# Optimization experiments

Hardware: AMD Instinct MI355X
Metric: run time of the kernel (lower is better)

## Reference

```python
import jax, jax.numpy as jnp
import numpy as np

B, T, C = 2048, 64, 384  # batch, seq (== block_size), n_embd
HEAD = 64


def setup_inputs() -> dict:
    key = jax.random.key(0)
    k1, k2, k3, k4 = jax.random.split(key, 4)
    x = jax.random.normal(k1, (B, T, C), dtype=jnp.float32)
    Wq = jax.random.normal(k2, (C, HEAD), dtype=jnp.float32) * (C ** -0.5)
    Wk = jax.random.normal(k3, (C, HEAD), dtype=jnp.float32) * (C ** -0.5)
    Wv = jax.random.normal(k4, (C, HEAD), dtype=jnp.float32) * (C ** -0.5)
    return {"x": x, "Wq": Wq, "Wk": Wk, "Wv": Wv}


def reference(x, Wq, Wk, Wv):
    Bx, Tx, Cx = x.shape
    q = jnp.einsum('btc,ch->bth', x, Wq)
    k = jnp.einsum('btc,ch->bth', x, Wk)
    v = jnp.einsum('btc,ch->bth', x, Wv)
    # NOTE: original code scales by n_embd**-0.5 (C), not head_size**-0.5
    wei = jnp.einsum('bth,bsh->bts', q, k) * (Cx ** -0.5)
    causal = jnp.tril(jnp.ones((Tx, Tx), dtype=bool))  # tril[:T,:T]
    wei = jnp.where(causal, wei, -jnp.inf)
    wei = jax.nn.softmax(wei, axis=-1)
    # dropout is identity in eval mode
    out = jnp.einsum('bts,bsh->bth', wei, v)
    return out
```

## Files before the change

kernel.cpp:

```cpp
#include <hip/hip_runtime.h>
#include <stdint.h>

typedef _Float16 f16;
typedef _Float16 f16x8 __attribute__((ext_vector_type(8)));
typedef _Float16 f16x4 __attribute__((ext_vector_type(4)));
typedef float floatx4 __attribute__((ext_vector_type(4)));
typedef float floatx2 __attribute__((ext_vector_type(2)));

#define TT 64
#define CDIM 384
#define HH 64
#define NKK 12
#define LDP 72
#define OST 66
#define CHUNK 12288
#define WBUFH 6144
#define ARENA 4608
#define SCALE 0.05103103630798288f

__global__ void prep_w(const float* __restrict__ Wq,
                       const float* __restrict__ Wk,
                       const float* __restrict__ Wv,
                       f16* __restrict__ wf) {
    int t = blockIdx.x * 256 + threadIdx.x;
    if (t >= 3 * NKK * 4 * 64) return;
    int lane = t & 63;
    int tile = (t >> 6) & 3;
    int p    = (t >> 8) % 3;
    int kk   = t / 768;
    const float* W = (p == 0) ? Wq : ((p == 1) ? Wk : Wv);
    int n  = tile * 16 + (lane & 15);
    int k0 = kk * 32 + (lane >> 4) * 8;
    f16x8 frag;
#pragma unroll
    for (int j = 0; j < 8; ++j) frag[j] = (f16)W[(k0 + j) * HH + n];
    ((f16x8*)wf)[t] = frag;
}

static __device__ __forceinline__ f16x8 cvt8(float4 f0, float4 f1) {
    f16x8 h;
    h[0]=(f16)f0.x; h[1]=(f16)f0.y; h[2]=(f16)f0.z; h[3]=(f16)f0.w;
    h[4]=(f16)f1.x; h[5]=(f16)f1.y; h[6]=(f16)f1.z; h[7]=(f16)f1.w;
    return h;
}

static __device__ __forceinline__ void glds16(const void* g, void* l) {
    __builtin_amdgcn_global_load_lds(
        (const __attribute__((address_space(1))) uint32_t*)g,
        (__attribute__((address_space(3))) uint32_t*)l, 16, 0, 0);
}

__launch_bounds__(256, 5)
__global__ void attn_head(const float* __restrict__ x,
                          const f16* __restrict__ wf,
                          float* __restrict__ out) {
    __shared__ __align__(16) char smem[3 * TT * LDP * sizeof(f16)];
    f16* wbuf = (f16*)smem;
    f16* qs   = (f16*)smem;
    f16* ksm  = qs + ARENA;
    f16* vst  = qs + 2 * ARENA;
    f16* ps   = qs;
    float* ost = (float*)smem;

    const int b    = blockIdx.x;
    const int tid  = threadIdx.x;
    const int wave = tid >> 6;
    const int lane = tid & 63;
    const int quad = lane >> 4;
    const int cl   = lane & 15;
    const int row0 = wave * 16;

    const floatx4 fzero = {0.f, 0.f, 0.f, 0.f};
    floatx4 acc[12];
#pragma unroll
    for (int T = 0; T < 12; ++T) acc[T] = fzero;

    const float* xp = x + ((size_t)b * TT + row0 + cl) * CDIM + quad * 8;
    const char* wb  = (const char*)wf;
    const int lslot = (wave * 64 + lane) * 16;

    float4 xa[2], xb[2];
#pragma unroll
    for (int j = 0; j < 3; ++j)
        glds16(wb + j * 4096 + lslot, wbuf + j * 2048 + wave * 512);
    asm volatile("" ::: "memory");
    xa[0] = *(const float4*)(xp);
    xb[0] = *(const float4*)(xp + 4);
    asm volatile("" ::: "memory");

#pragma unroll
    for (int kk = 0; kk < NKK; ++kk) {
        if (kk == NKK - 1) asm volatile("s_waitcnt vmcnt(0)" ::: "memory");
        else               asm volatile("s_waitcnt vmcnt(2)" ::: "memory");
        __builtin_amdgcn_s_barrier();
        if (kk + 1 < NKK) {
            const int nb = (kk + 1) & 1;
#pragma unroll
            for (int j = 0; j < 3; ++j)
                glds16(wb + (kk + 1) * CHUNK + j * 4096 + lslot,
                       wbuf + nb * WBUFH + j * 2048 + wave * 512);
            asm volatile("" ::: "memory");
            xa[nb] = *(const float4*)(xp + (kk + 1) * 32);
            xb[nb] = *(const float4*)(xp + (kk + 1) * 32 + 4);
            asm volatile("" ::: "memory");
        }
        f16x8 xf = cvt8(xa[kk & 1], xb[kk & 1]);
        const f16* wc = wbuf + (kk & 1) * WBUFH;
        __builtin_amdgcn_s_setprio(1);
#pragma unroll
        for (int T = 0; T < 12; ++T) {
            f16x8 bf = *(const f16x8*)&wc[(T * 64 + lane) * 8];
            acc[T] = __builtin_amdgcn_mfma_f32_16x16x32_f16(xf, bf, acc[T], 0, 0, 0);
        }
        __builtin_amdgcn_s_setprio(0);
    }
    __syncthreads();

#pragma unroll
    for (int T = 0; T < 12; ++T) {
        int p = T >> 2;
        int h = (T & 3) * 16 + cl;
        if (p == 2) {
            f16x4 vv;
            vv[0]=(f16)acc[T][0]; vv[1]=(f16)acc[T][1];
            vv[2]=(f16)acc[T][2]; vv[3]=(f16)acc[T][3];
            *(f16x4*)&vst[h * LDP + row0 + quad * 4] = vv;
        } else if (p == 0) {
#pragma unroll
            for (int r = 0; r < 4; ++r)
                qs[(row0 + quad * 4 + r) * LDP + h] = (f16)(acc[T][r] * SCALE);
        } else {
#pragma unroll
            for (int r = 0; r < 4; ++r)
                ksm[(row0 + quad * 4 + r) * LDP + h] = (f16)acc[T][r];
        }
    }
    __syncthreads();

    floatx4 sa[4];
#pragma unroll
    for (int t = 0; t < 4; ++t) sa[t] = fzero;
#pragma unroll
    for (int kv = 0; kv < 2; ++kv) {
        f16x8 aq = *(const f16x8*)&qs[(row0 + cl) * LDP + kv * 32 + quad * 8];
#pragma unroll
        for (int t = 0; t < 4; ++t) {
            f16x8 bk = *(const f16x8*)&ksm[(t * 16 + cl) * LDP + kv * 32 + quad * 8];
            sa[t] = __builtin_amdgcn_mfma_f32_16x16x32_f16(aq, bk, sa[t], 0, 0, 0);
        }
    }
    __syncthreads();

#pragma unroll
    for (int t = 0; t < 4; ++t) {
        int s = t * 16 + cl;
#pragma unroll
        for (int r = 0; r < 4; ++r) {
            int tr = row0 + quad * 4 + r;
            float p = (s <= tr) ? __expf(sa[t][r]) : 0.0f;
            ps[tr * LDP + s] = (f16)p;
        }
    }
    __syncthreads();

    floatx4 oa[4];
    floatx4 den = fzero;
#pragma unroll
    for (int t = 0; t < 4; ++t) oa[t] = fzero;
    f16x8 ones;
#pragma unroll
    for (int j = 0; j < 8; ++j) ones[j] = (f16)1.0f;
#pragma unroll
    for (int kv = 0; kv < 2; ++kv) {
        f16x8 ap = *(const f16x8*)&ps[(row0 + cl) * LDP + kv * 32 + quad * 8];
        den = __builtin_amdgcn_mfma_f32_16x16x32_f16(ap, ones, den, 0, 0, 0);
#pragma unroll
        for (int t = 0; t < 4; ++t) {
            f16x8 bv = *(const f16x8*)&vst[(t * 16 + cl) * LDP + kv * 32 + quad * 8];
            oa[t] = __builtin_amdgcn_mfma_f32_16x16x32_f16(ap, bv, oa[t], 0, 0, 0);
        }
    }
    float rden[4];
#pragma unroll
    for (int r = 0; r < 4; ++r) rden[r] = 1.0f / den[r];
    __syncthreads();

#pragma unroll
    for (int t = 0; t < 4; ++t)
#pragma unroll
        for (int r = 0; r < 4; ++r)
            ost[(row0 + quad * 4 + r) * OST + t * 16 + cl] = oa[t][r] * rden[r];
    __syncthreads();

    float* op = out + (size_t)b * TT * HH;
#pragma unroll
    for (int i = 0; i < 4; ++i) {
        int row = i * 16 + (tid >> 4);
        int c4  = (tid & 15) * 4;
        floatx2 lo = *(const floatx2*)&ost[row * OST + c4];
        floatx2 hi = *(const floatx2*)&ost[row * OST + c4 + 2];
        float4 v; v.x = lo[0]; v.y = lo[1]; v.z = hi[0]; v.w = hi[1];
        *(float4*)&op[row * HH + c4] = v;
    }
}

extern "C" void kernel_launch(void* const* d_in, const int* in_sizes, int n_in,
                              void* d_out, int out_size, void* d_ws, size_t ws_size,
                              hipStream_t stream) {
    const float* x  = (const float*)d_in[0];
    const float* Wq = (const float*)d_in[1];
    const float* Wk = (const float*)d_in[2];
    const float* Wv = (const float*)d_in[3];
    float* out = (float*)d_out;
    f16* wf = (f16*)d_ws;

    prep_w<<<36, 256, 0, stream>>>(Wq, Wk, Wv, wf);
    attn_head<<<2048, 256, 0, stream>>>(x, wf, out);
}
```

Before: 301.3 us.

## Load projection weights directly from global memory instead of LDS staging

New measurement: 330.8 us. 9.8% more time.

```diff
diff --git a/kernel.cpp b/kernel.cpp
--- a/kernel.cpp
+++ b/kernel.cpp
@@ -13,8 +13,6 @@
 #define NKK 12
 #define LDP 72
 #define OST 66
-#define CHUNK 12288
-#define WBUFH 6144
 #define ARENA 4608
 #define SCALE 0.05103103630798288f
 
@@ -44,18 +42,11 @@
     return h;
 }
 
-static __device__ __forceinline__ void glds16(const void* g, void* l) {
-    __builtin_amdgcn_global_load_lds(
-        (const __attribute__((address_space(1))) uint32_t*)g,
-        (__attribute__((address_space(3))) uint32_t*)l, 16, 0, 0);
-}
-
-__launch_bounds__(256, 5)
+__launch_bounds__(256, 4)
 __global__ void attn_head(const float* __restrict__ x,
                           const f16* __restrict__ wf,
                           float* __restrict__ out) {
     __shared__ __align__(16) char smem[3 * TT * LDP * sizeof(f16)];
-    f16* wbuf = (f16*)smem;
     f16* qs   = (f16*)smem;
     f16* ksm  = qs + ARENA;
     f16* vst  = qs + 2 * ARENA;
@@ -76,45 +67,25 @@
     for (int T = 0; T < 12; ++T) acc[T] = fzero;
 
     const float* xp = x + ((size_t)b * TT + row0 + cl) * CDIM + quad * 8;
-    const char* wb  = (const char*)wf;
-    const int lslot = (wave * 64 + lane) * 16;
+    const f16x8* wl = (const f16x8*)wf + lane;
 
-    float4 xa[2], xb[2];
-#pragma unroll
-    for (int j = 0; j < 3; ++j)
-        glds16(wb + j * 4096 + lslot, wbuf + j * 2048 + wave * 512);
-    asm volatile("" ::: "memory");
-    xa[0] = *(const float4*)(xp);
-    xb[0] = *(const float4*)(xp + 4);
-    asm volatile("" ::: "memory");
+    float4 xa = *(const float4*)(xp);
+    float4 xb = *(const float4*)(xp + 4);
 
-#pragma unroll
+#pragma unroll 2
     for (int kk = 0; kk < NKK; ++kk) {
-        if (kk == NKK - 1) asm volatile("s_waitcnt vmcnt(0)" ::: "memory");
-        else               asm volatile("s_waitcnt vmcnt(2)" ::: "memory");
-        __builtin_amdgcn_s_barrier();
+        f16x8 xf = cvt8(xa, xb);
         if (kk + 1 < NKK) {
-            const int nb = (kk + 1) & 1;
-#pragma unroll
-            for (int j = 0; j < 3; ++j)
-                glds16(wb + (kk + 1) * CHUNK + j * 4096 + lslot,
-                       wbuf + nb * WBUFH + j * 2048 + wave * 512);
-            asm volatile("" ::: "memory");
-            xa[nb] = *(const float4*)(xp + (kk + 1) * 32);
-            xb[nb] = *(const float4*)(xp + (kk + 1) * 32 + 4);
-            asm volatile("" ::: "memory");
+            xa = *(const float4*)(xp + (kk + 1) * 32);
+            xb = *(const float4*)(xp + (kk + 1) * 32 + 4);
         }
-        f16x8 xf = cvt8(xa[kk & 1], xb[kk & 1]);
-        const f16* wc = wbuf + (kk & 1) * WBUFH;
-        __builtin_amdgcn_s_setprio(1);
+        const f16x8* wk = wl + kk * 768;
 #pragma unroll
         for (int T = 0; T < 12; ++T) {
-            f16x8 bf = *(const f16x8*)&wc[(T * 64 + lane) * 8];
+            f16x8 bf = wk[T * 64];
             acc[T] = __builtin_amdgcn_mfma_f32_16x16x32_f16(xf, bf, acc[T], 0, 0, 0);
         }
-        __builtin_amdgcn_s_setprio(0);
     }
-    __syncthreads();
 
 #pragma unroll
     for (int T = 0; T < 12; ++T) {
@@ -149,7 +120,6 @@
             sa[t] = __builtin_amdgcn_mfma_f32_16x16x32_f16(aq, bk, sa[t], 0, 0, 0);
         }
     }
-    __syncthreads();
 
 #pragma unroll
     for (int t = 0; t < 4; ++t) {
@@ -161,7 +131,6 @@
             ps[tr * LDP + s] = (f16)p;
         }
     }
-    __syncthreads();
 
     floatx4 oa[4];
     floatx4 den = fzero;
```

## Split fused attention into QKV projection kernel and attention kernel via workspace

Applied to the files above, without the earlier changes.

Measured after the change: 329.1 us. +9.2%, slower.

```diff
diff --git a/kernel.cpp b/kernel.cpp
--- a/kernel.cpp
+++ b/kernel.cpp
@@ -5,18 +5,21 @@
 typedef _Float16 f16x8 __attribute__((ext_vector_type(8)));
 typedef _Float16 f16x4 __attribute__((ext_vector_type(4)));
 typedef float floatx4 __attribute__((ext_vector_type(4)));
-typedef float floatx2 __attribute__((ext_vector_type(2)));
 
 #define TT 64
 #define CDIM 384
 #define HH 64
 #define NKK 12
 #define LDP 72
-#define OST 66
 #define CHUNK 12288
 #define WBUFH 6144
-#define ARENA 4608
 #define SCALE 0.05103103630798288f
+
+#define WF_OFF 0
+#define QF_OFF (256 * 1024)
+#define TENB   (2048 * 64 * 64 * 2)
+#define KF_OFF (QF_OFF + TENB)
+#define VT_OFF (KF_OFF + TENB)
 
 __global__ void prep_w(const float* __restrict__ Wq,
                        const float* __restrict__ Wk,
@@ -50,17 +53,107 @@
         (__attribute__((address_space(3))) uint32_t*)l, 16, 0, 0);
 }
 
-__launch_bounds__(256, 5)
-__global__ void attn_head(const float* __restrict__ x,
-                          const f16* __restrict__ wf,
-                          float* __restrict__ out) {
-    __shared__ __align__(16) char smem[3 * TT * LDP * sizeof(f16)];
-    f16* wbuf = (f16*)smem;
-    f16* qs   = (f16*)smem;
-    f16* ksm  = qs + ARENA;
-    f16* vst  = qs + 2 * ARENA;
-    f16* ps   = qs;
-    float* ost = (float*)smem;
+__launch_bounds__(256, 3)
+__global__ void proj_qkv(const float* __restrict__ x,
+                         const f16* __restrict__ wf,
+                         f16* __restrict__ qf,
+                         f16* __restrict__ kf,
+                         f16* __restrict__ vt) {
+    __shared__ __align__(16) f16 wbuf[2 * WBUFH];
+
+    const int tid  = threadIdx.x;
+    const int wave = tid >> 6;
+    const int lane = tid & 63;
+    const int quad = lane >> 4;
+    const int cl   = lane & 15;
+    const int R0   = blockIdx.x * 128 + wave * 32;
+
+    const floatx4 fzero = {0.f, 0.f, 0.f, 0.f};
+    floatx4 acc[2][12];
+#pragma unroll
+    for (int mi = 0; mi < 2; ++mi)
+#pragma unroll
+        for (int T = 0; T < 12; ++T) acc[mi][T] = fzero;
+
+    const float* xp0 = x + (size_t)(R0 + cl) * CDIM + quad * 8;
+    const float* xp1 = x + (size_t)(R0 + 16 + cl) * CDIM + quad * 8;
+    const char*  wb  = (const char*)wf;
+    const int lslot  = (wave * 64 + lane) * 16;
+
+    float4 xa[2][2], xb[2][2];
+#pragma unroll
+    for (int j = 0; j < 3; ++j)
+        glds16(wb + j * 4096 + lslot, wbuf + j * 2048 + wave * 512);
+    asm volatile("" ::: "memory");
+    xa[0][0] = *(const float4*)(xp0); xb[0][0] = *(const float4*)(xp0 + 4);
+    xa[0][1] = *(const float4*)(xp1); xb[0][1] = *(const float4*)(xp1 + 4);
+    asm volatile("" ::: "memory");
+
+#pragma unroll
+    for (int kk = 0; kk < NKK; ++kk) {
+        asm volatile("s_waitcnt vmcnt(4)" ::: "memory");
+        __builtin_amdgcn_s_barrier();
+        if (kk + 1 < NKK) {
+            const int nb = (kk + 1) & 1;
+#pragma unroll
+            for (int j = 0; j < 3; ++j)
+                glds16(wb + (kk + 1) * CHUNK + j * 4096 + lslot,
+                       wbuf + nb * WBUFH + j * 2048 + wave * 512);
+            asm volatile("" ::: "memory");
+            xa[nb][0] = *(const float4*)(xp0 + (kk + 1) * 32);
+            xb[nb][0] = *(const float4*)(xp0 + (kk + 1) * 32 + 4);
+            xa[nb][1] = *(const float4*)(xp1 + (kk + 1) * 32);
+            xb[nb][1] = *(const float4*)(xp1 + (kk + 1) * 32 + 4);
+            asm volatile("" ::: "memory");
+        }
+        const int cur = kk & 1;
+        f16x8 xf0 = cvt8(xa[cur][0], xb[cur][0]);
+        f16x8 xf1 = cvt8(xa[cur][1], xb[cur][1]);
+        const f16* wc = wbuf + cur * WBUFH;
+        __builtin_amdgcn_s_setprio(1);
+#pragma unroll
+        for (int T = 0; T < 12; ++T) {
+            f16x8 bf = *(const f16x8*)&wc[(T * 64 + lane) * 8];
+            acc[0][T] = __builtin_amdgcn_mfma_f32_16x16x32_f16(xf0, bf, acc[0][T], 0, 0, 0);
+            acc[1][T] = __builtin_amdgcn_mfma_f32_16x16x32_f16(xf1, bf, acc[1][T], 0, 0, 0);
+        }
+        __builtin_amdgcn_s_setprio(0);
+    }
+
+#pragma unroll
+    for (int mi = 0; mi < 2; ++mi) {
+        const int rbase = R0 + mi * 16 + quad * 4;
+#pragma unroll
+        for (int T = 0; T < 12; ++T) {
+            const int p = T >> 2;
+            const int h = (T & 3) * 16 + cl;
+            if (p == 0) {
+#pragma unroll
+                for (int r = 0; r < 4; ++r)
+                    qf[(size_t)(rbase + r) * HH + h] = (f16)(acc[mi][T][r] * SCALE);
+            } else if (p == 1) {
+#pragma unroll
+                for (int r = 0; r < 4; ++r)
+                    kf[(size_t)(rbase + r) * HH + h] = (f16)acc[mi][T][r];
+            } else {
+                const int tb = R0 + mi * 16;
+                const int b  = tb >> 6;
+                const int t0 = (tb & 63) + quad * 4;
+                f16x4 vv;
+                vv[0]=(f16)acc[mi][T][0]; vv[1]=(f16)acc[mi][T][1];
+                vv[2]=(f16)acc[mi][T][2]; vv[3]=(f16)acc[mi][T][3];
+                *(f16x4*)&vt[(size_t)b * 4096 + h * 64 + t0] = vv;
+            }
+        }
+    }
+}
+
+__launch_bounds__(256, 4)
+__global__ void attn_sm(const f16* __restrict__ qf,
+                        const f16* __restrict__ kf,
+                        const f16* __restrict__ vt,
+                        float* __restrict__ out) {
+    __shared__ __align__(16) f16 ps[TT * LDP];
 
     const int b    = blockIdx.x;
     const int tid  = threadIdx.x;
@@ -69,87 +162,28 @@
     const int quad = lane >> 4;
     const int cl   = lane & 15;
     const int row0 = wave * 16;
+    const size_t base = (size_t)b * (TT * HH);
+
+    f16x8 aq[2], bk[4][2], bv[4][2];
+#pragma unroll
+    for (int kv = 0; kv < 2; ++kv) {
+        aq[kv] = *(const f16x8*)&qf[base + (row0 + cl) * HH + kv * 32 + quad * 8];
+#pragma unroll
+        for (int t = 0; t < 4; ++t) {
+            bk[t][kv] = *(const f16x8*)&kf[base + (t * 16 + cl) * HH + kv * 32 + quad * 8];
+            bv[t][kv] = *(const f16x8*)&vt[base + (t * 16 + cl) * HH + kv * 32 + quad * 8];
+        }
+    }
 
     const floatx4 fzero = {0.f, 0.f, 0.f, 0.f};
-    floatx4 acc[12];
-#pragma unroll
-    for (int T = 0; T < 12; ++T) acc[T] = fzero;
-
-    const float* xp = x + ((size_t)b * TT + row0 + cl) * CDIM + quad * 8;
-    const char* wb  = (const char*)wf;
-    const int lslot = (wave * 64 + lane) * 16;
-
-    float4 xa[2], xb[2];
-#pragma unroll
-    for (int j = 0; j < 3; ++j)
-        glds16(wb + j * 4096 + lslot, wbuf + j * 2048 + wave * 512);
-    asm volatile("" ::: "memory");
-    xa[0] = *(const float4*)(xp);
-    xb[0] = *(const float4*)(xp + 4);
-    asm volatile("" ::: "memory");
-
-#pragma unroll
-    for (int kk = 0; kk < NKK; ++kk) {
-        if (kk == NKK - 1) asm volatile("s_waitcnt vmcnt(0)" ::: "memory");
-        else               asm volatile("s_waitcnt vmcnt(2)" ::: "memory");
-        __builtin_amdgcn_s_barrier();
-        if (kk + 1 < NKK) {
-            const int nb = (kk + 1) & 1;
-#pragma unroll
-            for (int j = 0; j < 3; ++j)
-                glds16(wb + (kk + 1) * CHUNK + j * 4096 + lslot,
-                       wbuf + nb * WBUFH + j * 2048 + wave * 512);
-            asm volatile("" ::: "memory");
-            xa[nb] = *(const float4*)(xp + (kk + 1) * 32);
-            xb[nb] = *(const float4*)(xp + (kk + 1) * 32 + 4);
-            asm volatile("" ::: "memory");
-        }
-        f16x8 xf = cvt8(xa[kk & 1], xb[kk & 1]);
-        const f16* wc = wbuf + (kk & 1) * WBUFH;
-        __builtin_amdgcn_s_setprio(1);
-#pragma unroll
-        for (int T = 0; T < 12; ++T) {
-            f16x8 bf = *(const f16x8*)&wc[(T * 64 + lane) * 8];
-            acc[T] = __builtin_amdgcn_mfma_f32_16x16x32_f16(xf, bf, acc[T], 0, 0, 0);
-        }
-        __builtin_amdgcn_s_setprio(0);
-    }
-    __syncthreads();
-
-#pragma unroll
-    for (int T = 0; T < 12; ++T) {
-        int p = T >> 2;
-        int h = (T & 3) * 16 + cl;
-        if (p == 2) {
-            f16x4 vv;
-            vv[0]=(f16)acc[T][0]; vv[1]=(f16)acc[T][1];
-            vv[2]=(f16)acc[T][2]; vv[3]=(f16)acc[T][3];
-            *(f16x4*)&vst[h * LDP + row0 + quad * 4] = vv;
-        } else if (p == 0) {
-#pragma unroll
-            for (int r = 0; r < 4; ++r)
-                qs[(row0 + quad * 4 + r) * LDP + h] = (f16)(acc[T][r] * SCALE);
-        } else {
-#pragma unroll
-            for (int r = 0; r < 4; ++r)
-                ksm[(row0 + quad * 4 + r) * LDP + h] = (f16)acc[T][r];
-        }
-    }
-    __syncthreads();
-
     floatx4 sa[4];
 #pragma unroll
     for (int t = 0; t < 4; ++t) sa[t] = fzero;
 #pragma unroll
-    for (int kv = 0; kv < 2; ++kv) {
-        f16x8 aq = *(const f16x8*)&qs[(row0 + cl) * LDP + kv * 32 + quad * 8];
-#pragma unroll
-        for (int t = 0; t < 4; ++t) {
-            f16x8 bk = *(const f16x8*)&ksm[(t * 16 + cl) * LDP + kv * 32 + quad * 8];
-            sa[t] = __builtin_amdgcn_mfma_f32_16x16x32_f16(aq, bk, sa[t], 0, 0, 0);
-        }
-    }
-    __syncthreads();
+    for (int kv = 0; kv < 2; ++kv)
+#pragma unroll
+        for (int t = 0; t < 4; ++t)
+            sa[t] = __builtin_amdgcn_mfma_f32_16x16x32_f16(aq[kv], bk[t][kv], sa[t], 0, 0, 0);
 
 #pragma unroll
     for (int t = 0; t < 4; ++t) {
@@ -161,7 +195,6 @@
             ps[tr * LDP + s] = (f16)p;
         }
     }
-    __syncthreads();
 
     floatx4 oa[4];
     floatx4 den = fzero;
@@ -175,33 +208,19 @@
         f16x8 ap = *(const f16x8*)&ps[(row0 + cl) * LDP + kv * 32 + quad * 8];
         den = __builtin_amdgcn_mfma_f32_16x16x32_f16(ap, ones, den, 0, 0, 0);
 #pragma unroll
-        for (int t = 0; t < 4; ++t) {
-            f16x8 bv = *(const f16x8*)&vst[(t * 16 + cl) * LDP + kv * 32 + quad * 8];
-            oa[t] = __builtin_amdgcn_mfma_f32_16x16x32_f16(ap, bv, oa[t], 0, 0, 0);
-        }
+        for (int t = 0; t < 4; ++t)
+            oa[t] = __builtin_amdgcn_mfma_f32_16x16x32_f16(ap, bv[t][kv], oa[t], 0, 0, 0);
     }
     float rden[4];
 #pragma unroll
     for (int r = 0; r < 4; ++r) rden[r] = 1.0f / den[r];
-    __syncthreads();
-
+
+    float* op = out + base;
 #pragma unroll
     for (int t = 0; t < 4; ++t)
 #pragma unroll
         for (int r = 0; r < 4; ++r)
-            ost[(row0 + quad * 4 + r) * OST + t * 16 + cl] = oa[t][r] * rden[r];
-    __syncthreads();
-
-    float* op = out + (size_t)b * TT * HH;
-#pragma unroll
-    for (int i = 0; i < 4; ++i) {
-        int row = i * 16 + (tid >> 4);
-        int c4  = (tid & 15) * 4;
-        floatx2 lo = *(const floatx2*)&ost[row * OST + c4];
-        floatx2 hi = *(const floatx2*)&ost[row * OST + c4 + 2];
-        float4 v; v.x = lo[0]; v.y = lo[1]; v.z = hi[0]; v.w = hi[1];
-        *(float4*)&op[row * HH + c4] = v;
-    }
+            op[(row0 + quad * 4 + r) * HH + t * 16 + cl] = oa[t][r] * rden[r];
 }
 
 extern "C" void kernel_launch(void* const* d_in, const int* in_sizes, int n_in,
@@ -212,8 +231,13 @@
     const float* Wk = (const float*)d_in[2];
     const float* Wv = (const float*)d_in[3];
     float* out = (float*)d_out;
-    f16* wf = (f16*)d_ws;
+    char* ws = (char*)d_ws;
+    f16* wf = (f16*)(ws + WF_OFF);
+    f16* qf = (f16*)(ws + QF_OFF);
+    f16* kf = (f16*)(ws + KF_OFF);
+    f16* vt = (f16*)(ws + VT_OFF);
 
     prep_w<<<36, 256, 0, stream>>>(Wq, Wk, Wv, wf);
-    attn_head<<<2048, 256, 0, stream>>>(x, wf, out);
-}
+    proj_qkv<<<1024, 256, 0, stream>>>(x, wf, qf, kf, vt);
+    attn_sm<<<2048, 256, 0, stream>>>(qf, kf, vt, out);
+}
```

## Process two batches per 512-thread block and double the K step per stage

Applied to the files above, without the earlier changes.

Result: no change. 295.8 us (-1.8%).

```diff
diff --git a/kernel.cpp b/kernel.cpp
--- a/kernel.cpp
+++ b/kernel.cpp
@@ -10,11 +10,11 @@
 #define TT 64
 #define CDIM 384
 #define HH 64
-#define NKK 12
+#define NK2 6
 #define LDP 72
 #define OST 66
-#define CHUNK 12288
-#define WBUFH 6144
+#define CHUNK2 24576
+#define C2H 12288
 #define ARENA 4608
 #define SCALE 0.05103103630798288f
 
@@ -23,7 +23,7 @@
                        const float* __restrict__ Wv,
                        f16* __restrict__ wf) {
     int t = blockIdx.x * 256 + threadIdx.x;
-    if (t >= 3 * NKK * 4 * 64) return;
+    if (t >= 3 * 12 * 4 * 64) return;
     int lane = t & 63;
     int tile = (t >> 6) & 3;
     int p    = (t >> 8) % 3;
@@ -50,72 +50,83 @@
         (__attribute__((address_space(3))) uint32_t*)l, 16, 0, 0);
 }
 
-__launch_bounds__(256, 5)
+__launch_bounds__(512, 4)
 __global__ void attn_head(const float* __restrict__ x,
                           const f16* __restrict__ wf,
                           float* __restrict__ out) {
-    __shared__ __align__(16) char smem[3 * TT * LDP * sizeof(f16)];
+    __shared__ __align__(16) char smem[6 * ARENA * sizeof(f16)];
     f16* wbuf = (f16*)smem;
-    f16* qs   = (f16*)smem;
-    f16* ksm  = qs + ARENA;
-    f16* vst  = qs + 2 * ARENA;
-    f16* ps   = qs;
-    float* ost = (float*)smem;
-
-    const int b    = blockIdx.x;
+
+    const int b0   = blockIdx.x * 2;
     const int tid  = threadIdx.x;
     const int wave = tid >> 6;
     const int lane = tid & 63;
     const int quad = lane >> 4;
     const int cl   = lane & 15;
-    const int row0 = wave * 16;
+    const int bb   = wave >> 2;
+    const int row0b = (wave & 3) * 16;
 
     const floatx4 fzero = {0.f, 0.f, 0.f, 0.f};
     floatx4 acc[12];
 #pragma unroll
     for (int T = 0; T < 12; ++T) acc[T] = fzero;
 
-    const float* xp = x + ((size_t)b * TT + row0 + cl) * CDIM + quad * 8;
+    const float* xp = x + ((size_t)blockIdx.x * 128 + wave * 16 + cl) * CDIM + quad * 8;
     const char* wb  = (const char*)wf;
-    const int lslot = (wave * 64 + lane) * 16;
-
-    float4 xa[2], xb[2];
+
+    float4 xa[2][2], xb[2][2];
 #pragma unroll
     for (int j = 0; j < 3; ++j)
-        glds16(wb + j * 4096 + lslot, wbuf + j * 2048 + wave * 512);
+        glds16(wb + j * 8192 + tid * 16, wbuf + j * 4096 + wave * 512);
     asm volatile("" ::: "memory");
-    xa[0] = *(const float4*)(xp);
-    xb[0] = *(const float4*)(xp + 4);
+#pragma unroll
+    for (int s = 0; s < 2; ++s) {
+        xa[0][s] = *(const float4*)(xp + s * 32);
+        xb[0][s] = *(const float4*)(xp + s * 32 + 4);
+    }
     asm volatile("" ::: "memory");
 
 #pragma unroll
-    for (int kk = 0; kk < NKK; ++kk) {
-        if (kk == NKK - 1) asm volatile("s_waitcnt vmcnt(0)" ::: "memory");
-        else               asm volatile("s_waitcnt vmcnt(2)" ::: "memory");
+    for (int kk = 0; kk < NK2; ++kk) {
+        asm volatile("s_waitcnt vmcnt(4)" ::: "memory");
         __builtin_amdgcn_s_barrier();
-        if (kk + 1 < NKK) {
+        if (kk + 1 < NK2) {
             const int nb = (kk + 1) & 1;
 #pragma unroll
             for (int j = 0; j < 3; ++j)
-                glds16(wb + (kk + 1) * CHUNK + j * 4096 + lslot,
-                       wbuf + nb * WBUFH + j * 2048 + wave * 512);
+                glds16(wb + (kk + 1) * CHUNK2 + j * 8192 + tid * 16,
+                       wbuf + nb * C2H + j * 4096 + wave * 512);
             asm volatile("" ::: "memory");
-            xa[nb] = *(const float4*)(xp + (kk + 1) * 32);
-            xb[nb] = *(const float4*)(xp + (kk + 1) * 32 + 4);
+#pragma unroll
+            for (int s = 0; s < 2; ++s) {
+                xa[nb][s] = *(const float4*)(xp + (kk + 1) * 64 + s * 32);
+                xb[nb][s] = *(const float4*)(xp + (kk + 1) * 64 + s * 32 + 4);
+            }
             asm volatile("" ::: "memory");
         }
-        f16x8 xf = cvt8(xa[kk & 1], xb[kk & 1]);
-        const f16* wc = wbuf + (kk & 1) * WBUFH;
+        const int cur = kk & 1;
+        const f16* wc = wbuf + cur * C2H;
+        f16x8 xf0 = cvt8(xa[cur][0], xb[cur][0]);
+        f16x8 xf1 = cvt8(xa[cur][1], xb[cur][1]);
         __builtin_amdgcn_s_setprio(1);
 #pragma unroll
         for (int T = 0; T < 12; ++T) {
-            f16x8 bf = *(const f16x8*)&wc[(T * 64 + lane) * 8];
-            acc[T] = __builtin_amdgcn_mfma_f32_16x16x32_f16(xf, bf, acc[T], 0, 0, 0);
+            f16x8 bf0 = *(const f16x8*)&wc[(T * 64 + lane) * 8];
+            acc[T] = __builtin_amdgcn_mfma_f32_16x16x32_f16(xf0, bf0, acc[T], 0, 0, 0);
+        }
+#pragma unroll
+        for (int T = 0; T < 12; ++T) {
+            f16x8 bf1 = *(const f16x8*)&wc[6144 + (T * 64 + lane) * 8];
+            acc[T] = __builtin_amdgcn_mfma_f32_16x16x32_f16(xf1, bf1, acc[T], 0, 0, 0);
         }
         __builtin_amdgcn_s_setprio(0);
     }
     __syncthreads();
 
+    f16* qs  = (f16*)smem + bb * 3 * ARENA;
+    f16* ksm = qs + ARENA;
+    f16* vst = qs + 2 * ARENA;
+    f16* ps  = qs;
 #pragma unroll
     for (int T = 0; T < 12; ++T) {
         int p = T >> 2;
@@ -124,15 +135,15 @@
             f16x4 vv;
             vv[0]=(f16)acc[T][0]; vv[1]=(f16)acc[T][1];
             vv[2]=(f16)acc[T][2]; vv[3]=(f16)acc[T][3];
-            *(f16x4*)&vst[h * LDP + row0 + quad * 4] = vv;
+            *(f16x4*)&vst[h * LDP + row0b + quad * 4] = vv;
         } else if (p == 0) {
 #pragma unroll
             for (int r = 0; r < 4; ++r)
-                qs[(row0 + quad * 4 + r) * LDP + h] = (f16)(acc[T][r] * SCALE);
+                qs[(row0b + quad * 4 + r) * LDP + h] = (f16)(acc[T][r] * SCALE);
         } else {
 #pragma unroll
             for (int r = 0; r < 4; ++r)
-                ksm[(row0 + quad * 4 + r) * LDP + h] = (f16)acc[T][r];
+                ksm[(row0b + quad * 4 + r) * LDP + h] = (f16)acc[T][r];
         }
     }
     __syncthreads();
@@ -142,26 +153,24 @@
     for (int t = 0; t < 4; ++t) sa[t] = fzero;
 #pragma unroll
     for (int kv = 0; kv < 2; ++kv) {
-        f16x8 aq = *(const f16x8*)&qs[(row0 + cl) * LDP + kv * 32 + quad * 8];
+        f16x8 aq = *(const f16x8*)&qs[(row0b + cl) * LDP + kv * 32 + quad * 8];
 #pragma unroll
         for (int t = 0; t < 4; ++t) {
             f16x8 bk = *(const f16x8*)&ksm[(t * 16 + cl) * LDP + kv * 32 + quad * 8];
             sa[t] = __builtin_amdgcn_mfma_f32_16x16x32_f16(aq, bk, sa[t], 0, 0, 0);
         }
     }
-    __syncthreads();
 
 #pragma unroll
     for (int t = 0; t < 4; ++t) {
         int s = t * 16 + cl;
 #pragma unroll
         for (int r = 0; r < 4; ++r) {
-            int tr = row0 + quad * 4 + r;
+            int tr = row0b + quad * 4 + r;
             float p = (s <= tr) ? __expf(sa[t][r]) : 0.0f;
             ps[tr * LDP + s] = (f16)p;
         }
     }
-    __syncthreads();
 
     floatx4 oa[4];
     floatx4 den = fzero;
@@ -172,7 +181,7 @@
     for (int j = 0; j < 8; ++j) ones[j] = (f16)1.0f;
 #pragma unroll
     for (int kv = 0; kv < 2; ++kv) {
-        f16x8 ap = *(const f16x8*)&ps[(row0 + cl) * LDP + kv * 32 + quad * 8];
+        f16x8 ap = *(const f16x8*)&ps[(row0b + cl) * LDP + kv * 32 + quad * 8];
         den = __builtin_amdgcn_mfma_f32_16x16x32_f16(ap, ones, den, 0, 0, 0);
 #pragma unroll
         for (int t = 0; t < 4; ++t) {
@@ -185,20 +194,24 @@
     for (int r = 0; r < 4; ++r) rden[r] = 1.0f / den[r];
     __syncthreads();
 
+    float* ost = (float*)smem + bb * (TT * OST);
 #pragma unroll
     for (int t = 0; t < 4; ++t)
 #pragma unroll
         for (int r = 0; r < 4; ++r)
-            ost[(row0 + quad * 4 + r) * OST + t * 16 + cl] = oa[t][r] * rden[r];
-    __syncthreads();
-
-    float* op = out + (size_t)b * TT * HH;
+            ost[(row0b + quad * 4 + r) * OST + t * 16 + cl] = oa[t][r] * rden[r];
+    __syncthreads();
+
+    const int sb   = tid >> 8;
+    const int tid2 = tid & 255;
+    const float* osb = (const float*)smem + sb * (TT * OST);
+    float* op = out + ((size_t)b0 + sb) * TT * HH;
 #pragma unroll
     for (int i = 0; i < 4; ++i) {
-        int row = i * 16 + (tid >> 4);
-        int c4  = (tid & 15) * 4;
-        floatx2 lo = *(const floatx2*)&ost[row * OST + c4];
-        floatx2 hi = *(const floatx2*)&ost[row * OST + c4 + 2];
+        int row = i * 16 + (tid2 >> 4);
+        int c4  = (tid2 & 15) * 4;
+        floatx2 lo = *(const floatx2*)&osb[row * OST + c4];
+        floatx2 hi = *(const floatx2*)&osb[row * OST + c4 + 2];
         float4 v; v.x = lo[0]; v.y = lo[1]; v.z = hi[0]; v.w = hi[1];
         *(float4*)&op[row * HH + c4] = v;
     }
@@ -215,5 +228,5 @@
     f16* wf = (f16*)d_ws;
 
     prep_w<<<36, 256, 0, stream>>>(Wq, Wk, Wv, wf);
-    attn_head<<<2048, 256, 0, stream>>>(x, wf, out);
-}
+    attn_head<<<1024, 512, 0, stream>>>(x, wf, out);
+}
```
